# Kernel tuning notes

Measured on AMD Instinct MI355X. Metric: run time of the kernel, lower is better.

Reference implementation:

```python
import jax, jax.numpy as jnp
import numpy as np

KS, ST, PD = 4, 2, 1
AZI = 2.0 * np.pi / 1024.0
INC = 0.0073
C_IN, C_OUT = 64, 128


def _buffers():
    # torch: cos_azi[sh, sw] = cos(azi * (sw - ks//2)); cos_inc[sh, sw] = cos(inc * (sh - ks//2))
    d = np.arange(KS, dtype=np.float32) - KS // 2
    cos_azi = np.broadcast_to(np.cos(AZI * d)[None, :], (KS, KS))
    sin_azi = np.broadcast_to(np.sin(AZI * d)[None, :], (KS, KS))
    cos_inc = np.broadcast_to(np.cos(INC * d)[:, None], (KS, KS))
    sin_inc = np.broadcast_to(np.sin(INC * d)[:, None], (KS, KS))
    shp = (1, 1, 1, 1, KS, KS)
    return tuple(jnp.asarray(np.ascontiguousarray(b).reshape(shp), jnp.float32)
                 for b in (cos_azi, sin_azi, cos_inc, sin_inc))


def _pad(a, w_value):
    # pad width with constant, then height circularly (matches F.pad order in torch code)
    a = jnp.pad(a, ((0, 0), (0, 0), (0, 0), (PD, PD)), constant_values=w_value)
    return jnp.pad(a, ((0, 0), (0, 0), (PD, PD), (0, 0)), mode='wrap')


def _unfold(a):
    # torch a.unfold(3, ks, st).unfold(2, ks, st) -> [B,C,Ho,Wo,kw,kh]
    B, C, Hp, Wp = a.shape
    Ho = (Hp - KS) // ST + 1
    Wo = (Wp - KS) // ST + 1
    ih = (ST * jnp.arange(Ho))[:, None] + jnp.arange(KS)  # [Ho, ks]
    iw = (ST * jnp.arange(Wo))[:, None] + jnp.arange(KS)  # [Wo, ks]
    p = a[:, :, ih[:, None, :, None], iw[None, :, None, :]]  # [B,C,Ho,Wo,kh,kw]
    return jnp.transpose(p, (0, 1, 2, 3, 5, 4))               # [B,C,Ho,Wo,kw,kh]


def _forward(x, r, W1, b1, W2, b2, Wc, bc):
    cos_azi, sin_azi, cos_inc, sin_inc = _buffers()
    rp = _unfold(_pad(r, 100.0))                      # [B,1,Ho,Wo,kw,kh]
    r_center = rp[:, :, :, :, KS // 2, KS // 2]       # [B,1,Ho,Wo]
    pe0 = rp * cos_azi * cos_inc - r_center[..., None, None]
    pe1 = rp * cos_azi * sin_inc
    pe2 = rp * sin_azi
    pe = jnp.concatenate([pe0, pe1, pe2], axis=1)     # [B,3,Ho,Wo,kw,kh]
    pe = jnp.transpose(pe, (0, 2, 3, 4, 5, 1))        # [B,Ho,Wo,kw,kh,3]
    h = jax.nn.leaky_relu(pe @ W1 + b1, 0.2)          # [B,Ho,Wo,kw,kh,C]
    w = h @ W2 + b2                                   # [B,Ho,Wo,kw,kh,C]
    w = jnp.transpose(w, (0, 5, 1, 2, 3, 4))          # [B,C,Ho,Wo,kw,kh]
    xp = _unfold(_pad(x, 0.0)) * w                    # [B,C,Ho,Wo,kw,kh]
    B, C, Ho, Wo = xp.shape[:4]
    xp = jnp.transpose(xp, (0, 1, 4, 5, 2, 3)).reshape(B, C * KS * KS, Ho, Wo)
    out = jnp.einsum('bkhw,ok->bohw', xp, Wc) + bc[None, :, None, None]
    return out, r_center


def setup_inputs() -> dict:
    key = jax.random.key(0)
    ks = jax.random.split(key, 8)
    B, H, W = 4, 64, 1024
    x = jax.random.normal(ks[0], (B, C_IN, H, W), jnp.float32)
    r = jax.random.uniform(ks[1], (B, 1, H, W), jnp.float32) * 50.0  # metres
    W1 = jax.random.normal(ks[2], (3, C_IN), jnp.float32) * 0.3
    b1 = jax.random.normal(ks[3], (C_IN,), jnp.float32) * 0.02
    W2 = jax.random.normal(ks[4], (C_IN, C_IN), jnp.float32) * (1.0 / np.sqrt(C_IN))
    b2 = jax.random.normal(ks[5], (C_IN,), jnp.float32) * 0.02
    Wc = jax.random.normal(ks[6], (C_OUT, C_IN * KS * KS), jnp.float32) * (1.0 / np.sqrt(C_IN * KS * KS))
    bc = jax.random.normal(ks[7], (C_OUT,), jnp.float32) * 0.02
    return {'x': x, 'r': r, 'W1': W1, 'b1': b1, 'W2': W2, 'b2': b2, 'Wc': Wc, 'bc': bc}


def reference(x, r, W1, b1, W2, b2, Wc, bc):
    return _forward(x, r, W1, b1, W2, b2, Wc, bc)
```

## Files before the change

### kernel.cpp

```cpp
#include <hip/hip_runtime.h>
#include <hip/hip_bf16.h>

namespace {

constexpr int B_   = 4;
constexpr int CIN  = 64;
constexpr int COUT = 128;
constexpr int HIN  = 64,  WIN  = 1024;
constexpr int HOUT = 32,  WOUT = 512;
constexpr int TW   = 16;
constexpr int AB   = 1032;
constexpr int KTOT = CIN * 16;

typedef __bf16 bf16x8 __attribute__((ext_vector_type(8)));
typedef float  f32x4  __attribute__((ext_vector_type(4)));

__global__ void cvt_wc(const float* __restrict__ Wc, __hip_bfloat16* __restrict__ wcb, int n) {
    int i = blockIdx.x * 256 + threadIdx.x;
    if (i < n) wcb[i] = __float2bfloat16(Wc[i]);
}

__global__ __launch_bounds__(256, 4)
void fused_ccconv(const float* __restrict__ x,  const float* __restrict__ r,
                  const float* __restrict__ W1, const float* __restrict__ b1,
                  const float* __restrict__ W2, const float* __restrict__ b2,
                  const __hip_bfloat16* __restrict__ WcB,
                  const float* __restrict__ bc,
                  float* __restrict__ out)
{
    __shared__ __hip_bfloat16 A[TW * AB];

    const int t   = threadIdx.x;
    const int bx  = blockIdx.x;
    const int wt  = bx & 31;
    const int ho  = (bx >> 5) & 31;
    const int b   = bx >> 10;
    const int wo0 = wt * TW;

    const float* rb = r + (size_t)b * HIN * WIN;

    if (t < TW) {
        const int wo = wo0 + t;
        out[(size_t)B_*COUT*HOUT*WOUT + ((size_t)b*HOUT + ho)*WOUT + wo] =
            rb[(2*ho + 1)*WIN + (2*wo + 1)];
    }

    {
        const int p   = t >> 4;
        const int tap = t & 15;
        const int i   = tap >> 2;
        const int j   = tap & 3;
        const int wo  = wo0 + p;

        const float AZI = 0.006135923151542565f;
        const float INC = 0.0073f;
        const float di = (float)(i - 2);
        const float dj = (float)(j - 2);
        const float cA = cosf(AZI * dj), sA = sinf(AZI * dj);
        const float cI = cosf(INC * di), sI = sinf(INC * di);

        const int hsrc = (2*ho + j + 63) & 63;
        const int wsrc = 2*wo + i - 1;
        const bool inb = (unsigned)wsrc < (unsigned)WIN;

        const float rpv = inb ? rb[hsrc*WIN + wsrc] : 100.0f;
        const float rc  = rb[(2*ho + 1)*WIN + (2*wo + 1)];

        const float pe0 = rpv * cA * cI - rc;
        const float pe1 = rpv * cA * sI;
        const float pe2 = rpv * sA;

        float w[CIN];
        #pragma unroll
        for (int c = 0; c < CIN; ++c) w[c] = b2[c];

        for (int c1 = 0; c1 < CIN; ++c1) {
            float hv = fmaf(pe0, W1[c1],
                       fmaf(pe1, W1[CIN + c1],
                       fmaf(pe2, W1[2*CIN + c1], b1[c1])));
            hv = (hv >= 0.0f) ? hv : 0.2f * hv;
            const float* w2r = W2 + c1 * CIN;
            #pragma unroll
            for (int c = 0; c < CIN; ++c) w[c] = fmaf(hv, w2r[c], w[c]);
        }

        const float* xb = x + (size_t)b*CIN*HIN*WIN + hsrc*WIN + wsrc;
        __hip_bfloat16* Arow = A + p*AB + tap;
        #pragma unroll
        for (int c = 0; c < CIN; ++c) {
            const float xv = inb ? xb[(size_t)c * HIN * WIN] : 0.0f;
            Arow[c * 16] = __float2bfloat16(w[c] * xv);
        }
    }

    __syncthreads();

    const int wv   = t >> 6;
    const int ln   = t & 63;
    const int pcol = ln & 15;
    const int quad = ln >> 4;

    const int o0 = wv * 32;

    const __hip_bfloat16* wcP0 = WcB + ((size_t)(o0 + pcol)) * KTOT + quad*8;
    const __hip_bfloat16* wcP1 = wcP0 + (size_t)16 * KTOT;
    const __hip_bfloat16* aP   = A + pcol*AB + quad*8;

    f32x4 acc0 = {0.f,0.f,0.f,0.f};
    f32x4 acc1 = {0.f,0.f,0.f,0.f};

    #pragma unroll 4
    for (int ks = 0; ks < KTOT/32; ++ks) {
        const bf16x8 af = *reinterpret_cast<const bf16x8*>(aP   + ks*32);
        const bf16x8 w0 = *reinterpret_cast<const bf16x8*>(wcP0 + ks*32);
        const bf16x8 w1 = *reinterpret_cast<const bf16x8*>(wcP1 + ks*32);
        acc0 = __builtin_amdgcn_mfma_f32_16x16x32_bf16(w0, af, acc0, 0, 0, 0);
        acc1 = __builtin_amdgcn_mfma_f32_16x16x32_bf16(w1, af, acc1, 0, 0, 0);
    }

    #pragma unroll
    for (int q = 0; q < 4; ++q) {
        const int oa = o0 + quad*4 + q;
        const int ob = oa + 16;
        out[(((size_t)b*COUT + oa)*HOUT + ho)*WOUT + wo0 + pcol] = acc0[q] + bc[oa];
        out[(((size_t)b*COUT + ob)*HOUT + ho)*WOUT + wo0 + pcol] = acc1[q] + bc[ob];
    }
}

}

extern "C" void kernel_launch(void* const* d_in, const int* in_sizes, int n_in,
                              void* d_out, int out_size, void* d_ws, size_t ws_size,
                              hipStream_t stream) {
    const float* x  = (const float*)d_in[0];
    const float* r  = (const float*)d_in[1];
    const float* W1 = (const float*)d_in[2];
    const float* b1 = (const float*)d_in[3];
    const float* W2 = (const float*)d_in[4];
    const float* b2 = (const float*)d_in[5];
    const float* Wc = (const float*)d_in[6];
    const float* bc = (const float*)d_in[7];
    float* out = (float*)d_out;

    __hip_bfloat16* wcb = (__hip_bfloat16*)d_ws;
    const int nwc = COUT * KTOT;

    hipLaunchKernelGGL(cvt_wc, dim3((nwc + 255)/256), dim3(256), 0, stream, Wc, wcb, nwc);

    dim3 grid(B_ * HOUT * (WOUT / TW));
    dim3 block(256);
    hipLaunchKernelGGL(fused_ccconv, grid, block, 0, stream,
                       x, r, W1, b1, W2, b2, wcb, bc, out);
}
```

Before: 342.5 us.

## Compute W2 MLP layer with bf16 MFMA and reorder K layout tap-major

The per-tap 64x64 hidden-to-weight MLP layer, previously done with scalar FP32 FMAs per thread, now runs as bf16 MFMA tiles per wavefront. Results are staged in shared memory, then re-read per (pixel, tap) to form the x*w products. The Wc matrix is permuted in the prep kernel so the GEMM K dimension is tap-major, which allows packed 16-byte LDS writes. This removes most of the scalar FP32 work, at the cost of bf16 rounding of the hidden activations and weights, a larger shared buffer, and occupancy lowered to 3 blocks per SIMD.

```diff
diff --git a/kernel.cpp b/kernel.cpp
--- a/kernel.cpp
+++ b/kernel.cpp
@@ -9,26 +9,33 @@
 constexpr int HIN  = 64,  WIN  = 1024;
 constexpr int HOUT = 32,  WOUT = 512;
 constexpr int TW   = 16;
-constexpr int AB   = 1032;
+constexpr int SP   = 1096;
 constexpr int KTOT = CIN * 16;
 
 typedef __bf16 bf16x8 __attribute__((ext_vector_type(8)));
 typedef float  f32x4  __attribute__((ext_vector_type(4)));
 
-__global__ void cvt_wc(const float* __restrict__ Wc, __hip_bfloat16* __restrict__ wcb, int n) {
+__global__ void cvt_wts(const float* __restrict__ Wc, const float* __restrict__ W2,
+                        __hip_bfloat16* __restrict__ wcb, __hip_bfloat16* __restrict__ w2t) {
     int i = blockIdx.x * 256 + threadIdx.x;
-    if (i < n) wcb[i] = __float2bfloat16(Wc[i]);
-}
-
-__global__ __launch_bounds__(256, 4)
+    if (i < COUT * KTOT) {
+        int o = i >> 10, k = i & 1023, tap = k >> 6, c = k & 63;
+        wcb[i] = __float2bfloat16(Wc[(size_t)o * KTOT + c * 16 + tap]);
+    } else if (i < COUT * KTOT + CIN * CIN) {
+        int m = i - COUT * KTOT;
+        int c = m >> 6, c1 = m & 63;
+        w2t[m] = __float2bfloat16(W2[c1 * CIN + c]);
+    }
+}
+
+__global__ __launch_bounds__(256, 3)
 void fused_ccconv(const float* __restrict__ x,  const float* __restrict__ r,
                   const float* __restrict__ W1, const float* __restrict__ b1,
-                  const float* __restrict__ W2, const float* __restrict__ b2,
-                  const __hip_bfloat16* __restrict__ WcB,
-                  const float* __restrict__ bc,
+                  const __hip_bfloat16* __restrict__ W2T, const float* __restrict__ b2,
+                  const __hip_bfloat16* __restrict__ WcB, const float* __restrict__ bc,
                   float* __restrict__ out)
 {
-    __shared__ __hip_bfloat16 A[TW * AB];
+    __shared__ __hip_bfloat16 S[TW * SP];
 
     const int t   = threadIdx.x;
     const int bx  = blockIdx.x;
@@ -45,85 +52,142 @@
             rb[(2*ho + 1)*WIN + (2*wo + 1)];
     }
 
+    const int ln   = t & 63;
+    const int wv   = t >> 6;
+    const int lm   = ln & 15;
+    const int quad = ln >> 4;
+
+    const float AZI = 0.006135923151542565f;
+    const float INC = 0.0073f;
+
+    {
+        bf16x8 bfr[4][2];
+        float  b2v[4];
+        #pragma unroll
+        for (int nt = 0; nt < 4; ++nt) {
+            #pragma unroll
+            for (int ks = 0; ks < 2; ++ks)
+                bfr[nt][ks] = *reinterpret_cast<const bf16x8*>(
+                    W2T + (nt*16 + lm)*CIN + ks*32 + quad*8);
+            b2v[nt] = b2[nt*16 + lm];
+        }
+
+        const int i_ = lm >> 2, j_ = lm & 3;
+        const float di = (float)(i_ - 2), dj = (float)(j_ - 2);
+        const float cA = cosf(AZI * dj), sA = sinf(AZI * dj);
+        const float cI = cosf(INC * di), sI = sinf(INC * di);
+        const int hsrc = (2*ho + j_ + 63) & 63;
+
+        #pragma unroll
+        for (int mt = 0; mt < 4; ++mt) {
+            const int p  = wv*4 + mt;
+            const int wo = wo0 + p;
+            const int wsrc = 2*wo + i_ - 1;
+            const bool inb = (unsigned)wsrc < (unsigned)WIN;
+            const float rpv = inb ? rb[hsrc*WIN + wsrc] : 100.0f;
+            const float rc  = rb[(2*ho + 1)*WIN + (2*wo + 1)];
+            const float pe0 = rpv * cA * cI - rc;
+            const float pe1 = rpv * cA * sI;
+            const float pe2 = rpv * sA;
+
+            bf16x8 af0, af1;
+            #pragma unroll
+            for (int ks = 0; ks < 2; ++ks) {
+                const int cb = ks*32 + quad*8;
+                #pragma unroll
+                for (int j = 0; j < 8; ++j) {
+                    const int c1 = cb + j;
+                    float hv = fmaf(pe0, W1[c1],
+                               fmaf(pe1, W1[CIN + c1],
+                               fmaf(pe2, W1[2*CIN + c1], b1[c1])));
+                    hv = (hv >= 0.0f) ? hv : 0.2f * hv;
+                    __hip_bfloat16 hb = __float2bfloat16(hv);
+                    if (ks == 0) af0[j] = *reinterpret_cast<__bf16*>(&hb);
+                    else         af1[j] = *reinterpret_cast<__bf16*>(&hb);
+                }
+            }
+
+            #pragma unroll
+            for (int nt = 0; nt < 4; ++nt) {
+                f32x4 acc = {b2v[nt], b2v[nt], b2v[nt], b2v[nt]};
+                acc = __builtin_amdgcn_mfma_f32_16x16x32_bf16(af0, bfr[nt][0], acc, 0, 0, 0);
+                acc = __builtin_amdgcn_mfma_f32_16x16x32_bf16(af1, bfr[nt][1], acc, 0, 0, 0);
+                #pragma unroll
+                for (int q = 0; q < 4; ++q)
+                    S[p*SP + (quad*4 + q)*68 + nt*16 + lm] = __float2bfloat16(acc[q]);
+            }
+        }
+    }
+
     {
         const int p   = t >> 4;
         const int tap = t & 15;
-        const int i   = tap >> 2;
-        const int j   = tap & 3;
-        const int wo  = wo0 + p;
-
-        const float AZI = 0.006135923151542565f;
-        const float INC = 0.0073f;
-        const float di = (float)(i - 2);
-        const float dj = (float)(j - 2);
-        const float cA = cosf(AZI * dj), sA = sinf(AZI * dj);
-        const float cI = cosf(INC * di), sI = sinf(INC * di);
-
-        const int hsrc = (2*ho + j + 63) & 63;
-        const int wsrc = 2*wo + i - 1;
+        const int i_  = tap >> 2, j_ = tap & 3;
+        const int hsrc = (2*ho + j_ + 63) & 63;
+        const int wo   = wo0 + p;
+        const int wsrc = 2*wo + i_ - 1;
         const bool inb = (unsigned)wsrc < (unsigned)WIN;
 
-        const float rpv = inb ? rb[hsrc*WIN + wsrc] : 100.0f;
-        const float rc  = rb[(2*ho + 1)*WIN + (2*wo + 1)];
-
-        const float pe0 = rpv * cA * cI - rc;
-        const float pe1 = rpv * cA * sI;
-        const float pe2 = rpv * sA;
-
-        float w[CIN];
-        #pragma unroll
-        for (int c = 0; c < CIN; ++c) w[c] = b2[c];
-
-        for (int c1 = 0; c1 < CIN; ++c1) {
-            float hv = fmaf(pe0, W1[c1],
-                       fmaf(pe1, W1[CIN + c1],
-                       fmaf(pe2, W1[2*CIN + c1], b1[c1])));
-            hv = (hv >= 0.0f) ? hv : 0.2f * hv;
-            const float* w2r = W2 + c1 * CIN;
-            #pragma unroll
-            for (int c = 0; c < CIN; ++c) w[c] = fmaf(hv, w2r[c], w[c]);
-        }
+        uint2 wrow[16];
+        const uint2* wp = reinterpret_cast<const uint2*>(S + p*SP + tap*68);
+        #pragma unroll
+        for (int u = 0; u < 16; ++u) wrow[u] = wp[u];
 
         const float* xb = x + (size_t)b*CIN*HIN*WIN + hsrc*WIN + wsrc;
-        __hip_bfloat16* Arow = A + p*AB + tap;
-        #pragma unroll
-        for (int c = 0; c < CIN; ++c) {
-            const float xv = inb ? xb[(size_t)c * HIN * WIN] : 0.0f;
-            Arow[c * 16] = __float2bfloat16(w[c] * xv);
+
+        float xall[CIN];
+        #pragma unroll
+        for (int c = 0; c < CIN; ++c)
+            xall[c] = inb ? xb[(size_t)c * HIN * WIN] : 0.0f;
+
+        uint4* Ap = reinterpret_cast<uint4*>(S + p*SP + tap*64);
+        #pragma unroll
+        for (int g = 0; g < 8; ++g) {
+            uint pk[4];
+            #pragma unroll
+            for (int pr = 0; pr < 4; ++pr) {
+                const int c0 = g*8 + pr*2;
+                const uint2 wv2 = wrow[c0 >> 2];
+                const uint word = (c0 & 2) ? wv2.y : wv2.x;
+                const float w0 = __uint_as_float(word << 16);
+                const float w1 = __uint_as_float(word & 0xffff0000u);
+                __hip_bfloat16 p0 = __float2bfloat16(w0 * xall[c0]);
+                __hip_bfloat16 p1 = __float2bfloat16(w1 * xall[c0 + 1]);
+                const uint lo = *reinterpret_cast<unsigned short*>(&p0);
+                const uint hi = *reinterpret_cast<unsigned short*>(&p1);
+                pk[pr] = lo | (hi << 16);
+            }
+            Ap[g] = make_uint4(pk[0], pk[1], pk[2], pk[3]);
         }
     }
 
     __syncthreads();
 
-    const int wv   = t >> 6;
-    const int ln   = t & 63;
-    const int pcol = ln & 15;
-    const int quad = ln >> 4;
-
-    const int o0 = wv * 32;
-
-    const __hip_bfloat16* wcP0 = WcB + ((size_t)(o0 + pcol)) * KTOT + quad*8;
-    const __hip_bfloat16* wcP1 = wcP0 + (size_t)16 * KTOT;
-    const __hip_bfloat16* aP   = A + pcol*AB + quad*8;
-
-    f32x4 acc0 = {0.f,0.f,0.f,0.f};
-    f32x4 acc1 = {0.f,0.f,0.f,0.f};
-
-    #pragma unroll 4
-    for (int ks = 0; ks < KTOT/32; ++ks) {
-        const bf16x8 af = *reinterpret_cast<const bf16x8*>(aP   + ks*32);
-        const bf16x8 w0 = *reinterpret_cast<const bf16x8*>(wcP0 + ks*32);
-        const bf16x8 w1 = *reinterpret_cast<const bf16x8*>(wcP1 + ks*32);
-        acc0 = __builtin_amdgcn_mfma_f32_16x16x32_bf16(w0, af, acc0, 0, 0, 0);
-        acc1 = __builtin_amdgcn_mfma_f32_16x16x32_bf16(w1, af, acc1, 0, 0, 0);
-    }
-
-    #pragma unroll
-    for (int q = 0; q < 4; ++q) {
-        const int oa = o0 + quad*4 + q;
-        const int ob = oa + 16;
-        out[(((size_t)b*COUT + oa)*HOUT + ho)*WOUT + wo0 + pcol] = acc0[q] + bc[oa];
-        out[(((size_t)b*COUT + ob)*HOUT + ho)*WOUT + wo0 + pcol] = acc1[q] + bc[ob];
+    {
+        const int o0 = wv * 32;
+        const __hip_bfloat16* wcP0 = WcB + ((size_t)(o0 + lm)) * KTOT + quad*8;
+        const __hip_bfloat16* wcP1 = wcP0 + (size_t)16 * KTOT;
+        const __hip_bfloat16* aP   = S + lm*SP + quad*8;
+
+        f32x4 acc0 = {0.f,0.f,0.f,0.f};
+        f32x4 acc1 = {0.f,0.f,0.f,0.f};
+
+        #pragma unroll 4
+        for (int ks = 0; ks < KTOT/32; ++ks) {
+            const bf16x8 af = *reinterpret_cast<const bf16x8*>(aP   + ks*32);
+            const bf16x8 w0 = *reinterpret_cast<const bf16x8*>(wcP0 + ks*32);
+            const bf16x8 w1 = *reinterpret_cast<const bf16x8*>(wcP1 + ks*32);
+            acc0 = __builtin_amdgcn_mfma_f32_16x16x32_bf16(w0, af, acc0, 0, 0, 0);
+            acc1 = __builtin_amdgcn_mfma_f32_16x16x32_bf16(w1, af, acc1, 0, 0, 0);
+        }
+
+        #pragma unroll
+        for (int q = 0; q < 4; ++q) {
+            const int oa = o0 + quad*4 + q;
+            const int ob = oa + 16;
+            out[(((size_t)b*COUT + oa)*HOUT + ho)*WOUT + wo0 + lm] = acc0[q] + bc[oa];
+            out[(((size_t)b*COUT + ob)*HOUT + ho)*WOUT + wo0 + lm] = acc1[q] + bc[ob];
+        }
     }
 }
 
@@ -143,12 +207,14 @@
     float* out = (float*)d_out;
 
     __hip_bfloat16* wcb = (__hip_bfloat16*)d_ws;
-    const int nwc = COUT * KTOT;
-
-    hipLaunchKernelGGL(cvt_wc, dim3((nwc + 255)/256), dim3(256), 0, stream, Wc, wcb, nwc);
+    __hip_bfloat16* w2t = (__hip_bfloat16*)((char*)d_ws + 262144);
+
+    const int ntot = COUT*KTOT + CIN*CIN;
+    hipLaunchKernelGGL(cvt_wts, dim3((ntot + 255)/256), dim3(256), 0, stream,
+                       Wc, W2, wcb, w2t);
 
     dim3 grid(B_ * HOUT * (WOUT / TW));
     dim3 block(256);
     hipLaunchKernelGGL(fused_ccconv, grid, block, 0, stream,
-                       x, r, W1, b1, W2, b2, wcb, bc, out);
-}
+                       x, r, W1, b1, w2t, b2, wcb, bc, out);
+}
```

Result: faster. 289.2 us (-15.6%).
